# Optimization experiments

Hardware: AMD Instinct MI355X
Metric: run time of the kernel (lower is better)

## Reference

```python
import jax, jax.numpy as jnp
import numpy as np

SCALE = 1.0  # Scaler(scale=1.0) is a fixed multiplicative scale


def setup_inputs() -> dict:
    key = jax.random.key(0)
    ks = jax.random.split(key, 7)
    d = 2048          # in_features == out_features (per-head proj dim)
    out_total = 3 * d # fused QKV weight rows
    r = 8             # LoRA rank
    B, S = 4, 2048
    return {
        "x": jax.random.normal(ks[0], (B, S, d), dtype=jnp.float32),
        "W": jax.random.normal(ks[1], (out_total, d), dtype=jnp.float32) * 0.02,
        "b": jax.random.normal(ks[2], (out_total,), dtype=jnp.float32) * 0.02,
        "A1": jax.random.normal(ks[3], (r, d), dtype=jnp.float32) * 0.02,
        "B1": jax.random.normal(ks[4], (d, r), dtype=jnp.float32) * 0.02,
        "A2": jax.random.normal(ks[5], (r, d), dtype=jnp.float32) * 0.02,
        "B2": jax.random.normal(ks[6], (d, r), dtype=jnp.float32) * 0.02,
    }


def reference(x, W, b, A1, B1, A2, B2):
    # Low-rank deltas for K and V rows: each [out_features, in_features]
    dK = SCALE * (B1 @ A1)            # [d, d]
    dV = SCALE * (B2 @ A2)            # [d, d]
    delta = jnp.concatenate([dK, dV], axis=0)          # [2d, d]
    # zero-pad on top to match full fused weight (Q rows untouched)
    pad_rows = W.shape[0] - delta.shape[0]
    delta_full = jnp.concatenate(
        [jnp.zeros((pad_rows, W.shape[1]), dtype=W.dtype), delta], axis=0
    )                                                    # [3d, d]
    weight = W + delta_full
    # F.linear: x @ weight.T + b
    return jnp.einsum("bsd,od->bso", x, weight) + b
```

## Files before the change

### kernel.cpp

```cpp
#include <hip/hip_runtime.h>
#include <hip/hip_bf16.h>
#include <stdint.h>
#include <stddef.h>

typedef __attribute__((ext_vector_type(8)))  __bf16 bf16x8;
typedef __attribute__((ext_vector_type(16))) float  f32x16;
typedef __attribute__((ext_vector_type(8)))  unsigned short ushort8;

typedef const void __attribute__((address_space(1)))* as1_cvp;
typedef void       __attribute__((address_space(3)))* as3_vp;

__device__ __forceinline__ void gload_lds16(const void* g, void* l) {
    __builtin_amdgcn_global_load_lds((as1_cvp)g, (as3_vp)l, 16, 0, 0);
}

__device__ __forceinline__ unsigned short f2bf(float f) {
    union { float f; unsigned u; } v; v.f = f;
    unsigned r = v.u + 0x7fffu + ((v.u >> 16) & 1u);
    return (unsigned short)(r >> 16);
}

__global__ __launch_bounds__(256) void prep_kernel(
    const float* __restrict__ x,
    const float* __restrict__ W,
    const float* __restrict__ A1, const float* __restrict__ B1,
    const float* __restrict__ A2, const float* __restrict__ B2,
    unsigned short* __restrict__ Xb, unsigned short* __restrict__ Wb,
    int d, int nW, int n8)
{
    int blk = blockIdx.x;
    if (blk < nW) {
        int o  = blk;
        int k0 = threadIdx.x * 8;
        const float4* wrow = (const float4*)(W + (size_t)o * d + k0);
        float4 w0 = wrow[0], w1 = wrow[1];
        float acc[8] = {w0.x, w0.y, w0.z, w0.w, w1.x, w1.y, w1.z, w1.w};
        if (o >= d) {
            const float* A  = (o < 2 * d) ? A1 : A2;
            const float* Bm = (o < 2 * d) ? B1 : B2;
            int r0 = o - ((o < 2 * d) ? d : 2 * d);
#pragma unroll
            for (int r = 0; r < 8; ++r) {
                float bb = Bm[(size_t)r0 * 8 + r];
                const float4* arow = (const float4*)(A + (size_t)r * d + k0);
                float4 a0 = arow[0], a1 = arow[1];
                acc[0] += bb * a0.x; acc[1] += bb * a0.y;
                acc[2] += bb * a0.z; acc[3] += bb * a0.w;
                acc[4] += bb * a1.x; acc[5] += bb * a1.y;
                acc[6] += bb * a1.z; acc[7] += bb * a1.w;
            }
        }
        ushort8 ov;
#pragma unroll
        for (int c = 0; c < 8; ++c) ov[c] = f2bf(acc[c]);
        ((ushort8*)(Wb + (size_t)o * d))[threadIdx.x] = ov;
    } else {
        int i = (blk - nW) * 256 + threadIdx.x;
        if (i >= n8) return;
        const float4* s = (const float4*)x + (size_t)i * 2;
        float4 a = s[0], c = s[1];
        ushort8 o;
        o[0] = f2bf(a.x); o[1] = f2bf(a.y); o[2] = f2bf(a.z); o[3] = f2bf(a.w);
        o[4] = f2bf(c.x); o[5] = f2bf(c.y); o[6] = f2bf(c.z); o[7] = f2bf(c.w);
        ((ushort8*)Xb)[i] = o;
    }
}

constexpr int BM = 128, BN = 128, BK = 64;

__global__ __launch_bounds__(256) void gemm_bt_kernel(
    const unsigned short* __restrict__ Xb,
    const unsigned short* __restrict__ Wb,
    const float* __restrict__ bias,
    float* __restrict__ out,
    int M, int N, int K)
{
    __shared__ __align__(16) unsigned short As[BM * BK];
    __shared__ __align__(16) unsigned short Bs[BN * BK];

    const int tid  = threadIdx.x;
    const int wave = tid >> 6;
    const int lane = tid & 63;
    const int half = lane >> 5;
    const int ln32 = lane & 31;

    const int bm = blockIdx.y * BM;
    const int bn = blockIdx.x * BN;

    const int m0 = tid >> 3;
    const int c0 = (tid & 7) ^ (m0 & 7);
    const size_t goff = (size_t)m0 * K + c0 * 8;

    const int wm = (wave & 1) * 64;
    const int wn = (wave >> 1) * 64;

    const int r7 = ln32 & 7;
    int dofs[4];
#pragma unroll
    for (int s = 0; s < 4; ++s) dofs[s] = ((s * 2 + half) ^ r7) * 8;
    int baseA[2], baseB[2];
#pragma unroll
    for (int i = 0; i < 2; ++i) {
        baseA[i] = (wm + i * 32 + ln32) * 64;
        baseB[i] = (wn + i * 32 + ln32) * 64;
    }

    f32x16 acc[2][2];
#pragma unroll
    for (int i = 0; i < 2; ++i)
#pragma unroll
        for (int j = 0; j < 2; ++j)
#pragma unroll
            for (int r = 0; r < 16; ++r) acc[i][j][r] = 0.f;

    for (int kt = 0; kt < K; kt += BK) {
        const unsigned short* pa = Xb + (size_t)bm * K + kt + goff;
        const unsigned short* pb = Wb + (size_t)bn * K + kt + goff;
#pragma unroll
        for (int t = 0; t < 4; ++t) {
            gload_lds16(pa + (size_t)t * 32 * K, &As[(t * 256 + wave * 64) * 8]);
            gload_lds16(pb + (size_t)t * 32 * K, &Bs[(t * 256 + wave * 64) * 8]);
        }
        __syncthreads();

#pragma unroll
        for (int s = 0; s < 4; ++s) {
            bf16x8 a0 = *(const bf16x8*)&As[baseA[0] + dofs[s]];
            bf16x8 a1 = *(const bf16x8*)&As[baseA[1] + dofs[s]];
            bf16x8 b0 = *(const bf16x8*)&Bs[baseB[0] + dofs[s]];
            bf16x8 b1 = *(const bf16x8*)&Bs[baseB[1] + dofs[s]];
            acc[0][0] = __builtin_amdgcn_mfma_f32_32x32x16_bf16(a0, b0, acc[0][0], 0, 0, 0);
            acc[0][1] = __builtin_amdgcn_mfma_f32_32x32x16_bf16(a0, b1, acc[0][1], 0, 0, 0);
            acc[1][0] = __builtin_amdgcn_mfma_f32_32x32x16_bf16(a1, b0, acc[1][0], 0, 0, 0);
            acc[1][1] = __builtin_amdgcn_mfma_f32_32x32x16_bf16(a1, b1, acc[1][1], 0, 0, 0);
        }
        __syncthreads();
    }

#pragma unroll
    for (int j = 0; j < 2; ++j) {
        int col = bn + wn + j * 32 + ln32;
        float bv = bias[col];
#pragma unroll
        for (int i = 0; i < 2; ++i) {
            int rbase = bm + wm + i * 32 + 4 * half;
#pragma unroll
            for (int reg = 0; reg < 16; ++reg) {
                int row = rbase + (reg & 3) + 8 * (reg >> 2);
                out[(size_t)row * N + col] = acc[i][j][reg] + bv;
            }
        }
    }
}

extern "C" void kernel_launch(void* const* d_in, const int* in_sizes, int n_in,
                              void* d_out, int out_size, void* d_ws, size_t ws_size,
                              hipStream_t stream) {
    const float* x  = (const float*)d_in[0];
    const float* W  = (const float*)d_in[1];
    const float* b  = (const float*)d_in[2];
    const float* A1 = (const float*)d_in[3];
    const float* B1 = (const float*)d_in[4];
    const float* A2 = (const float*)d_in[5];
    const float* B2 = (const float*)d_in[6];
    float* out = (float*)d_out;

    const int d = 2048;
    const int K = d;
    const int N = 3 * d;
    const int M = in_sizes[0] / d;

    unsigned short* Xbf = (unsigned short*)d_ws;
    unsigned short* Wbf = Xbf + (size_t)M * K;

    int n8 = (M * K) / 8;
    int castBlocks = (n8 + 255) / 256;
    prep_kernel<<<N + castBlocks, 256, 0, stream>>>(x, W, A1, B1, A2, B2,
                                                    Xbf, Wbf, d, N, n8);

    dim3 grid(N / BN, M / BM);
    gemm_bt_kernel<<<grid, 256, 0, stream>>>(Xbf, Wbf, b, out, M, N, K);
}
```

Measured before the change: 496.2 us.

## Rewrite GEMM with 256x256 tiles, double-buffered LDS and interleaved prefetch

Replaces the 128x128 single-buffered GEMM with a 256x256-tile, 8-wave kernel that double-buffers LDS and issues the next tiles' global-to-LDS loads in chunks between MFMA clusters. Each cluster runs at raised wave priority, and manual vmcnt waits and barriers replace the per-iteration syncthreads. A 1D grid with an XCD-aware block swizzle improves L2 locality. The gains sought are more data reuse per tile and latency hiding of loads, at the cost of higher register and LDS use (128KB LDS per block at 2 blocks per CU) and hardcoded K/N dimensions.

```diff
diff --git a/kernel.cpp b/kernel.cpp
--- a/kernel.cpp
+++ b/kernel.cpp
@@ -66,88 +66,149 @@
     }
 }
 
-constexpr int BM = 128, BN = 128, BK = 64;
-
-__global__ __launch_bounds__(256) void gemm_bt_kernel(
+constexpr int BM = 256, BN = 256, BK = 64;
+constexpr int KK = 2048, NN = 6144;
+constexpr int TT = KK / BK;
+
+__global__ __launch_bounds__(512, 2) void gemm256_kernel(
     const unsigned short* __restrict__ Xb,
     const unsigned short* __restrict__ Wb,
     const float* __restrict__ bias,
     float* __restrict__ out,
-    int M, int N, int K)
+    int M)
 {
-    __shared__ __align__(16) unsigned short As[BM * BK];
-    __shared__ __align__(16) unsigned short Bs[BN * BK];
+    __shared__ __align__(16) unsigned short As[2][BM * BK];
+    __shared__ __align__(16) unsigned short Bs[2][BN * BK];
 
     const int tid  = threadIdx.x;
     const int wave = tid >> 6;
     const int lane = tid & 63;
     const int half = lane >> 5;
     const int ln32 = lane & 31;
-
-    const int bm = blockIdx.y * BM;
-    const int bn = blockIdx.x * BN;
-
-    const int m0 = tid >> 3;
-    const int c0 = (tid & 7) ^ (m0 & 7);
-    const size_t goff = (size_t)m0 * K + c0 * 8;
-
-    const int wm = (wave & 1) * 64;
-    const int wn = (wave >> 1) * 64;
+    const int wrow = wave >> 2;
+    const int wcol = wave & 3;
+
+    int nwg = (int)gridDim.x;
+    int bid = (int)blockIdx.x;
+    int swz = bid;
+    if ((nwg & 7) == 0) swz = (bid & 7) * (nwg >> 3) + (bid >> 3);
+    const int ntn = NN / BN;
+    const int bm = (swz / ntn) * BM;
+    const int bn = (swz % ntn) * BN;
+
+    const int rtid = tid >> 3;
+    const int ctid = (tid & 7) ^ (rtid & 7);
+    const size_t gA0 = (size_t)(bm + rtid) * KK + ctid * 8;
+    const size_t gB0 = (size_t)(bn + rtid) * KK + ctid * 8;
+    const int ldsW = wave * 512;
+
+#define STAGE_A(t, j, buf) gload_lds16(Xb + gA0 + (size_t)(j) * 64 * KK + (size_t)(t) * BK, \
+                                       &As[(buf)][(j) * 4096 + ldsW])
+#define STAGE_B(t, j, buf) gload_lds16(Wb + gB0 + (size_t)(j) * 64 * KK + (size_t)(t) * BK, \
+                                       &Bs[(buf)][(j) * 4096 + ldsW])
 
     const int r7 = ln32 & 7;
     int dofs[4];
 #pragma unroll
     for (int s = 0; s < 4; ++s) dofs[s] = ((s * 2 + half) ^ r7) * 8;
-    int baseA[2], baseB[2];
-#pragma unroll
-    for (int i = 0; i < 2; ++i) {
-        baseA[i] = (wm + i * 32 + ln32) * 64;
-        baseB[i] = (wn + i * 32 + ln32) * 64;
-    }
-
-    f32x16 acc[2][2];
-#pragma unroll
-    for (int i = 0; i < 2; ++i)
+    int baseA[2][2];
+#pragma unroll
+    for (int qm = 0; qm < 2; ++qm)
+#pragma unroll
+        for (int f = 0; f < 2; ++f)
+            baseA[qm][f] = (wrow * 128 + qm * 64 + f * 32 + ln32) * BK;
+    int baseB[2];
+#pragma unroll
+    for (int qn = 0; qn < 2; ++qn) baseB[qn] = (wcol * 64 + qn * 32 + ln32) * BK;
+
+    f32x16 acc[4][2];
+#pragma unroll
+    for (int i = 0; i < 4; ++i)
 #pragma unroll
         for (int j = 0; j < 2; ++j)
 #pragma unroll
             for (int r = 0; r < 16; ++r) acc[i][j][r] = 0.f;
 
-    for (int kt = 0; kt < K; kt += BK) {
-        const unsigned short* pa = Xb + (size_t)bm * K + kt + goff;
-        const unsigned short* pb = Wb + (size_t)bn * K + kt + goff;
-#pragma unroll
-        for (int t = 0; t < 4; ++t) {
-            gload_lds16(pa + (size_t)t * 32 * K, &As[(t * 256 + wave * 64) * 8]);
-            gload_lds16(pb + (size_t)t * 32 * K, &Bs[(t * 256 + wave * 64) * 8]);
-        }
-        __syncthreads();
-
-#pragma unroll
-        for (int s = 0; s < 4; ++s) {
-            bf16x8 a0 = *(const bf16x8*)&As[baseA[0] + dofs[s]];
-            bf16x8 a1 = *(const bf16x8*)&As[baseA[1] + dofs[s]];
-            bf16x8 b0 = *(const bf16x8*)&Bs[baseB[0] + dofs[s]];
-            bf16x8 b1 = *(const bf16x8*)&Bs[baseB[1] + dofs[s]];
-            acc[0][0] = __builtin_amdgcn_mfma_f32_32x32x16_bf16(a0, b0, acc[0][0], 0, 0, 0);
-            acc[0][1] = __builtin_amdgcn_mfma_f32_32x32x16_bf16(a0, b1, acc[0][1], 0, 0, 0);
-            acc[1][0] = __builtin_amdgcn_mfma_f32_32x32x16_bf16(a1, b0, acc[1][0], 0, 0, 0);
-            acc[1][1] = __builtin_amdgcn_mfma_f32_32x32x16_bf16(a1, b1, acc[1][1], 0, 0, 0);
-        }
-        __syncthreads();
-    }
+    bf16x8 a[2][4], b0[4], b1[4];
+
+#define LOAD_A(qm) do { _Pragma("unroll") for (int s = 0; s < 4; ++s) {        \
+        a[0][s] = *(const bf16x8*)&Aq[baseA[qm][0] + dofs[s]];                 \
+        a[1][s] = *(const bf16x8*)&Aq[baseA[qm][1] + dofs[s]]; } } while (0)
+#define LOAD_B(qn, BB) do { _Pragma("unroll") for (int s = 0; s < 4; ++s) {    \
+        BB[s] = *(const bf16x8*)&Bq[baseB[qn] + dofs[s]]; } } while (0)
+#define MFMA_CL(i0, i1, jj, BB) do {                                           \
+        __builtin_amdgcn_s_setprio(1);                                         \
+        _Pragma("unroll") for (int s = 0; s < 4; ++s) {                        \
+            acc[i0][jj] = __builtin_amdgcn_mfma_f32_32x32x16_bf16(a[0][s], BB[s], acc[i0][jj], 0, 0, 0); \
+            acc[i1][jj] = __builtin_amdgcn_mfma_f32_32x32x16_bf16(a[1][s], BB[s], acc[i1][jj], 0, 0, 0); \
+        }                                                                      \
+        __builtin_amdgcn_s_setprio(0); } while (0)
+#define BAR() asm volatile("s_barrier" ::: "memory")
+
+#define GROUP(v, SN1, SN2, VMW) do {                                           \
+        const int q_ = (v) & 1;                                                \
+        const unsigned short* Aq = &As[q_][0];                                 \
+        const unsigned short* Bq = &Bs[q_][0];                                 \
+                                                                      \
+        LOAD_A(0); LOAD_B(0, b0);                                              \
+        if (SN1) { STAGE_B((v) + 1, 2, q_ ^ 1); STAGE_B((v) + 1, 3, q_ ^ 1); } \
+        BAR();                                                                 \
+        MFMA_CL(0, 1, 0, b0);                                                  \
+        BAR();                                                                 \
+                                                                      \
+        LOAD_B(1, b1);                                                         \
+        if (SN1) { STAGE_A((v) + 1, 1, q_ ^ 1); STAGE_A((v) + 1, 3, q_ ^ 1); } \
+        BAR();                                                                 \
+        MFMA_CL(0, 1, 1, b1);                                                  \
+        BAR();                                                                 \
+                                                                      \
+        LOAD_A(1);                                                             \
+        if (SN2) { STAGE_A((v) + 2, 0, q_); STAGE_A((v) + 2, 2, q_); }         \
+        BAR();                                                                 \
+        MFMA_CL(2, 3, 0, b0);                                                  \
+        BAR();                                                                 \
+                                                                      \
+        if (SN2) { STAGE_B((v) + 2, 0, q_); STAGE_B((v) + 2, 1, q_); }         \
+        if ((VMW) == 4)      asm volatile("s_waitcnt vmcnt(4)" ::: "memory");  \
+        else if ((VMW) == 0) asm volatile("s_waitcnt vmcnt(0)" ::: "memory");  \
+        BAR();                                                                 \
+        MFMA_CL(2, 3, 1, b1);                                                  \
+        BAR();                                                                 \
+    } while (0)
+
+#pragma unroll
+    for (int j = 0; j < 4; ++j) STAGE_A(0, j, 0);
+#pragma unroll
+    for (int j = 0; j < 4; ++j) STAGE_B(0, j, 0);
+    STAGE_A(1, 0, 1); STAGE_A(1, 2, 1);
+    STAGE_B(1, 0, 1); STAGE_B(1, 1, 1);
+    asm volatile("s_waitcnt vmcnt(4)" ::: "memory");
+    BAR();
+
+#pragma unroll 2
+    for (int v = 0; v < TT - 2; ++v) GROUP(v, 1, 1, 4);
+    GROUP(TT - 2, 1, 0, 0);
+    GROUP(TT - 1, 0, 0, -1);
+
+#undef GROUP
+#undef BAR
+#undef MFMA_CL
+#undef LOAD_B
+#undef LOAD_A
+#undef STAGE_B
+#undef STAGE_A
 
 #pragma unroll
     for (int j = 0; j < 2; ++j) {
-        int col = bn + wn + j * 32 + ln32;
+        int col = bn + wcol * 64 + j * 32 + ln32;
         float bv = bias[col];
 #pragma unroll
-        for (int i = 0; i < 2; ++i) {
-            int rbase = bm + wm + i * 32 + 4 * half;
+        for (int i = 0; i < 4; ++i) {
+            int rbase = bm + wrow * 128 + i * 32 + 4 * half;
 #pragma unroll
             for (int reg = 0; reg < 16; ++reg) {
                 int row = rbase + (reg & 3) + 8 * (reg >> 2);
-                out[(size_t)row * N + col] = acc[i][j][reg] + bv;
+                out[(size_t)row * NN + col] = acc[i][j][reg] + bv;
             }
         }
     }
@@ -178,6 +239,6 @@
     prep_kernel<<<N + castBlocks, 256, 0, stream>>>(x, W, A1, B1, A2, B2,
                                                     Xbf, Wbf, d, N, n8);
 
-    dim3 grid(N / BN, M / BM);
-    gemm_bt_kernel<<<grid, 256, 0, stream>>>(Xbf, Wbf, b, out, M, N, K);
-}
+    dim3 grid((M / BM) * (N / BN));
+    gemm256_kernel<<<grid, 512, 0, stream>>>(Xbf, Wbf, b, out, M);
+}
```

Result: faster. 484.7 us (-2.3%).
